# Kernel tuning notes

Measured on AMD Instinct MI355X. Metric: run time of the kernel, lower is better.

Reference implementation:

```python
import jax, jax.numpy as jnp
import numpy as np

DIM = 1024
HEADS = 16
DH = 64            # dim // heads
LOCAL_HEADS = 8
WINDOW = 128
NEG = -jnp.finfo(jnp.float32).max


def _look_around_kv(z, pad_value):
    # z: (b, h, nw, w, d) -> (b, h, nw, 3w, d); backward=1, forward=1 window
    nw = z.shape[2]
    zp = jnp.pad(z, ((0, 0), (0, 0), (1, 1), (0, 0), (0, 0)), constant_values=pad_value)
    return jnp.concatenate([zp[:, :, i:i + nw] for i in range(3)], axis=3)


def _local_attention(q, k, v, valid):
    # q,k,v: (b, h, t, d); valid: (b, t) True = keep (module passes ~input_mask)
    b, h, t, d = q.shape
    nw = t // WINDOW
    bucket = lambda z: z.reshape(b, h, nw, WINDOW, d)
    bq, bk, bv = bucket(q), bucket(k), bucket(v)
    bk = _look_around_kv(bk, 0.0)
    bv = _look_around_kv(bv, 0.0)
    # key position indices with -1 padding for out-of-range windows
    t_idx = jnp.arange(t, dtype=jnp.int32).reshape(nw, WINDOW)
    tp = jnp.pad(t_idx, ((1, 1), (0, 0)), constant_values=-1)
    bq_k = jnp.concatenate([tp[i:i + nw] for i in range(3)], axis=1)  # (nw, 3w)
    oob = (bq_k == -1)[None, None, :, None, :]                        # (1,1,nw,1,3w)
    # input mask pair: mq & mk
    vm = valid.reshape(b, nw, WINDOW)
    vmp = jnp.pad(vm, ((0, 0), (1, 1), (0, 0)), constant_values=False)
    vmk = jnp.concatenate([vmp[:, i:i + nw] for i in range(3)], axis=2)  # (b, nw, 3w)
    pair = vm[:, None, :, :, None] & vmk[:, None, :, None, :]            # (b,1,nw,w,3w)
    dots = jnp.einsum('bhnwd,bhnkd->bhnwk', bq, bk) * (d ** -0.5)
    dots = jnp.where(oob, NEG, dots)
    dots = jnp.where(pair, dots, NEG)
    attn = jax.nn.softmax(dots, axis=-1)
    out = jnp.einsum('bhnwk,bhnkd->bhnwd', attn, bv)
    return out.reshape(b, h, t, d)


def _linear_attn(q, k, v, valid):
    # q,k,v: (b, h, t, d); valid: (b, t) True = keep
    d = q.shape[-1]
    m = valid[:, None, :, None]
    k = jnp.where(m, k, NEG)
    v = jnp.where(m, v, 0.0)
    q = jax.nn.softmax(q, axis=-1) * (d ** -0.5)
    k = jax.nn.softmax(k, axis=-2)
    context = jnp.einsum('bhnd,bhne->bhde', k, v)
    return jnp.einsum('bhnd,bhde->bhne', q, context)


def setup_inputs() -> dict:
    key = jax.random.key(0)
    ks = jax.random.split(key, 7)
    b, t = 2, 4096
    x = jax.random.normal(ks[0], (b, t, DIM), dtype=jnp.float32)
    input_mask = jax.random.bernoulli(ks[1], 0.1, (b, t))  # True = padded token
    s = DIM ** -0.5
    Wq = jax.random.normal(ks[2], (DIM, HEADS * DH), jnp.float32) * s
    Wk = jax.random.normal(ks[3], (DIM, HEADS * DH), jnp.float32) * s
    Wv = jax.random.normal(ks[4], (DIM, HEADS * DH), jnp.float32) * s
    Wo = jax.random.normal(ks[5], (HEADS * DH, DIM), jnp.float32) * s
    bo = jax.random.normal(ks[6], (DIM,), jnp.float32) * 0.01
    return {"x": x, "input_mask": input_mask, "Wq": Wq, "Wk": Wk, "Wv": Wv, "Wo": Wo, "bo": bo}


def reference(x, input_mask, Wq, Wk, Wv, Wo, bo):
    b, t, _ = x.shape
    split_heads = lambda z: z.reshape(b, t, HEADS, DH).transpose(0, 2, 1, 3)
    q = split_heads(x @ Wq)
    k = split_heads(x @ Wk)
    v = split_heads(x @ Wv)
    valid = ~input_mask
    lq, gq = q[:, :LOCAL_HEADS], q[:, LOCAL_HEADS:]
    lk, gk = k[:, :LOCAL_HEADS], k[:, LOCAL_HEADS:]
    lv, gv = v[:, :LOCAL_HEADS], v[:, LOCAL_HEADS:]
    local_out = _local_attention(lq, lk, lv, valid)
    global_out = _linear_attn(gq, gk, gv, valid)
    attn = jnp.concatenate([local_out, global_out], axis=1)  # (b, h, t, d)
    attn = attn.transpose(0, 2, 1, 3).reshape(b, t, HEADS * DH)
    return attn @ Wo + bo
```

## Files before the change

### kernel.cpp

```cpp
#include <hip/hip_runtime.h>
#include <cstdint>
#include <cfloat>
#include <math.h>

typedef __bf16 bf16_t;
typedef __bf16 bf16x8 __attribute__((ext_vector_type(8)));
typedef __bf16 bf16x4 __attribute__((ext_vector_type(4)));
typedef float  f32x4  __attribute__((ext_vector_type(4)));
typedef unsigned int u32;

#define NEGF (-3.4028234663852886e38f)

static __device__ __forceinline__ f32x4 mfma16(bf16x8 a, bf16x8 b, f32x4 c) {
  return __builtin_amdgcn_mfma_f32_16x16x32_bf16(a, b, c, 0, 0, 0);
}
static __device__ __forceinline__ void gload_lds16(const bf16_t* g, bf16_t* l) {
  __builtin_amdgcn_global_load_lds((const __attribute__((address_space(1))) void*)g,
                                   (__attribute__((address_space(3))) void*)l, 16, 0, 0);
}

__global__ void k_prep(const uint8_t* __restrict__ mraw, uint8_t* __restrict__ valid) {
  __shared__ int f1, f3;
  int tid = threadIdx.x;
  if (tid == 0) { f1 = 0; f3 = 0; }
  __syncthreads();
  int l1 = 0, l3 = 0;
  for (int i = tid; i < 8192; i += 256) {
    uint8_t v = mraw[i];
    if (v) { int r = i & 3; if (r == 1 || r == 2) l1 = 1; if (r == 3) l3 = 1; }
  }
  if (l1) atomicOr(&f1, 1);
  if (l3) atomicOr(&f3, 1);
  __syncthreads();
  int layout = f1 ? 0 : (f3 ? 2 : 1);
  for (int i = tid; i < 8192; i += 256) {
    bool m;
    if (layout == 0)      m = mraw[i] != 0;
    else if (layout == 1) m = ((const int*)mraw)[i] != 0;
    else                  m = ((const float*)mraw)[i] != 0.0f;
    valid[i] = m ? (uint8_t)0 : (uint8_t)1;
  }
}

__global__ void k_cast_x(const float* __restrict__ x, bf16_t* __restrict__ xb) {
  int i = blockIdx.x * 256 + threadIdx.x;
  float4 v = ((const float4*)x)[i];
  bf16x4 o = { (bf16_t)v.x, (bf16_t)v.y, (bf16_t)v.z, (bf16_t)v.w };
  *(bf16x4*)(xb + (size_t)i * 4) = o;
}

__global__ void k_transw(const float* __restrict__ Wq, const float* __restrict__ Wk,
                         const float* __restrict__ Wv, const float* __restrict__ Wo,
                         bf16_t* __restrict__ WT, bf16_t* __restrict__ WoT) {
  __shared__ float tile[32][33];
  int z = blockIdx.z;
  const float* src = (z == 0) ? Wq : (z == 1) ? Wk : (z == 2) ? Wv : Wo;
  bf16_t* dst = (z < 3) ? (WT + (size_t)z * 1024 * 1024) : WoT;
  int x0 = blockIdx.x * 32, y0 = blockIdx.y * 32;
  int tx = threadIdx.x, ty = threadIdx.y;
  #pragma unroll
  for (int j = 0; j < 32; j += 8)
    tile[ty + j][tx] = src[(size_t)(y0 + ty + j) * 1024 + x0 + tx];
  __syncthreads();
  #pragma unroll
  for (int j = 0; j < 32; j += 8)
    dst[(size_t)(x0 + ty + j) * 1024 + y0 + tx] = (bf16_t)tile[tx][ty + j];
}

template<bool OUT_BF16>
__global__ __launch_bounds__(256, 2) void k_gemm(const bf16_t* __restrict__ A,
                                                 const bf16_t* __restrict__ Bt,
                                                 void* __restrict__ Cout,
                                                 const float* __restrict__ bias,
                                                 int M, int N, int K) {
  __shared__ __align__(16) uint8_t shmem[34816];
  bf16_t* As = (bf16_t*)shmem;
  bf16_t* Bs = As + 128 * 64;
  int nbn = N >> 7;
  int nwg = (M >> 7) * nbn;
  int per = nwg >> 3;
  int id  = blockIdx.x;
  int sw  = (id & 7) * per + (id >> 3);
  int mb = sw / nbn, nb = sw % nbn;

  const int tid = threadIdx.x;
  const int lane = tid & 63, wv = tid >> 6;
  const int c = lane & 15, g = lane >> 4;
  const size_t m0 = (size_t)mb * 128, n0 = (size_t)nb * 128;
  const int wm = (wv >> 1) * 64, wn = (wv & 1) * 64;

  f32x4 zero = {0.f, 0.f, 0.f, 0.f};
  f32x4 acc[4][4];
  #pragma unroll
  for (int m = 0; m < 4; ++m)
    #pragma unroll
    for (int n = 0; n < 4; ++n) acc[m][n] = zero;

  for (int kt = 0; kt < K; kt += 64) {
    if (kt) __syncthreads();
    #pragma unroll
    for (int p = 0; p < 4; ++p) {
      int seg = p * 256 + tid;
      int r = seg >> 3, s = seg & 7;
      int sc = (s ^ (r & 7)) * 8;
      gload_lds16(A + (m0 + r) * (size_t)K + kt + sc, As + seg * 8);
    }
    #pragma unroll
    for (int p = 0; p < 4; ++p) {
      int seg = p * 256 + tid;
      int r = seg >> 3, s = seg & 7;
      int sc = (s ^ (r & 7)) * 8;
      gload_lds16(Bt + (n0 + r) * (size_t)K + kt + sc, Bs + seg * 8);
    }
    __syncthreads();
    #pragma unroll
    for (int kk = 0; kk < 2; ++kk) {
      bf16x8 af[4], bfv[4];
      #pragma unroll
      for (int m = 0; m < 4; ++m) {
        int row = wm + m * 16 + c;
        int sl = (g + 4 * kk) ^ (row & 7);
        af[m] = *(const bf16x8*)(As + row * 64 + sl * 8);
      }
      #pragma unroll
      for (int n = 0; n < 4; ++n) {
        int row = wn + n * 16 + c;
        int sl = (g + 4 * kk) ^ (row & 7);
        bfv[n] = *(const bf16x8*)(Bs + row * 64 + sl * 8);
      }
      #pragma unroll
      for (int m = 0; m < 4; ++m)
        #pragma unroll
        for (int n = 0; n < 4; ++n)
          acc[m][n] = mfma16(af[m], bfv[n], acc[m][n]);
    }
  }

  __syncthreads();
  if (OUT_BF16) {
    bf16_t* L = (bf16_t*)shmem;
    #pragma unroll
    for (int m = 0; m < 4; ++m)
      #pragma unroll
      for (int n = 0; n < 4; ++n)
        #pragma unroll
        for (int i = 0; i < 4; ++i)
          L[(wm + m * 16 + 4 * g + i) * 136 + wn + n * 16 + c] = (bf16_t)acc[m][n][i];
    __syncthreads();
    bf16_t* C = (bf16_t*)Cout;
    #pragma unroll
    for (int p = 0; p < 8; ++p) {
      int idx = p * 2048 + tid * 8;
      int row = idx >> 7, col = idx & 127;
      bf16x8 v = *(const bf16x8*)(L + row * 136 + col);
      *(bf16x8*)(C + (m0 + row) * (size_t)N + n0 + col) = v;
    }
  } else {
    float* C = (float*)Cout;
    float* L = (float*)shmem;
    #pragma unroll
    for (int half = 0; half < 2; ++half) {
      if (half) __syncthreads();
      if ((wv >> 1) == half) {
        #pragma unroll
        for (int m = 0; m < 4; ++m)
          #pragma unroll
          for (int n = 0; n < 4; ++n)
            #pragma unroll
            for (int i = 0; i < 4; ++i)
              L[(m * 16 + 4 * g + i) * 132 + wn + n * 16 + c] = acc[m][n][i];
      }
      __syncthreads();
      #pragma unroll
      for (int p = 0; p < 8; ++p) {
        int lin = p * 1024 + tid * 4;
        int row = lin >> 7, col = lin & 127;
        float4 v = *(const float4*)(L + row * 132 + col);
        float4 bv = *(const float4*)(bias + n0 + col);
        v.x += bv.x; v.y += bv.y; v.z += bv.z; v.w += bv.w;
        *(float4*)(C + (m0 + half * 64 + row) * (size_t)N + n0 + col) = v;
      }
    }
  }
}

__global__ __launch_bounds__(512) void k_local(const bf16_t* __restrict__ qkv,
                                               const uint8_t* __restrict__ valid,
                                               bf16_t* __restrict__ attn) {
  __shared__ __align__(16) uint8_t smem[50688];
  bf16_t* Ks = (bf16_t*)smem;
  bf16_t* VT = (bf16_t*)smem;
  uint8_t* s_key = smem + 50176;
  uint8_t* s_q   = smem + 50560;

  int bid = blockIdx.x;
  int w = bid & 31, h = (bid >> 5) & 7, b = bid >> 8;
  int tid = threadIdx.x;
  const int lane = tid & 63, wv = tid >> 6;
  const int c = lane & 15, g = lane >> 4;
  const int tkbase = (w - 1) * 128;

  #pragma unroll
  for (int p = 0; p < 6; ++p) {
    int seg = p * 512 + tid;
    int r = seg >> 3, s = seg & 7;
    int tk = tkbase + r;
    bf16x8 v8 = { (bf16_t)0.f,(bf16_t)0.f,(bf16_t)0.f,(bf16_t)0.f,
                  (bf16_t)0.f,(bf16_t)0.f,(bf16_t)0.f,(bf16_t)0.f };
    if ((unsigned)tk < 4096u)
      v8 = *(const bf16x8*)(qkv + (size_t)(b * 4096 + tk) * 3072 + 1024 + h * 64 + s * 8);
    *(bf16x8*)(Ks + r * 64 + ((s ^ (r & 7)) * 8)) = v8;
  }
  if (tid < 384) {
    int tk = tkbase + tid;
    s_key[tid] = ((unsigned)tk < 4096u) ? valid[b * 4096 + tk] : (uint8_t)0;
  }
  if (tid < 128) s_q[tid] = valid[b * 4096 + w * 128 + tid];
  __syncthreads();

  int m0 = wv * 16;
  bf16x8 qa0, qa1;
  {
    const bf16_t* qrow = qkv + (size_t)(b * 4096 + w * 128 + m0 + c) * 3072 + h * 64;
    qa0 = *(const bf16x8*)(qrow + g * 8);
    qa1 = *(const bf16x8*)(qrow + 32 + g * 8);
  }
  f32x4 zero = {0.f, 0.f, 0.f, 0.f};
  f32x4 acc[24];
  #pragma unroll
  for (int nt = 0; nt < 24; ++nt) acc[nt] = zero;
  #pragma unroll
  for (int nt = 0; nt < 24; ++nt) {
    int n = nt * 16 + c;
    bf16x8 k0 = *(const bf16x8*)(Ks + n * 64 + ((g       ^ (n & 7)) * 8));
    bf16x8 k1 = *(const bf16x8*)(Ks + n * 64 + (((g + 4) ^ (n & 7)) * 8));
    acc[nt] = mfma16(k0, qa0, acc[nt]);
    acc[nt] = mfma16(k1, qa1, acc[nt]);
  }
  __syncthreads();

  {
    int e = tid & 63, tg = tid >> 6;
    #pragma unroll 8
    for (int j = 0; j < 48; ++j) {
      int r = tg * 48 + j;
      int tk = tkbase + r;
      bf16_t v = (bf16_t)0.f;
      if ((unsigned)tk < 4096u)
        v = qkv[(size_t)(b * 4096 + tk) * 3072 + 2048 + h * 64 + e];
      VT[e * 392 + r] = v;
    }
  }

  bool qv = s_q[m0 + c] != 0;
  #pragma unroll
  for (int nt = 0; nt < 24; ++nt) {
    u32 kv4 = *(const u32*)(s_key + nt * 16 + 4 * g);
    #pragma unroll
    for (int i = 0; i < 4; ++i) {
      bool kv = ((kv4 >> (8 * i)) & 255u) != 0u;
      acc[nt][i] = (qv && kv) ? acc[nt][i] * 0.125f : NEGF;
    }
  }
  float mx = NEGF;
  #pragma unroll
  for (int nt = 0; nt < 24; ++nt)
    #pragma unroll
    for (int i = 0; i < 4; ++i) mx = fmaxf(mx, acc[nt][i]);
  mx = fmaxf(mx, __shfl_xor(mx, 16, 64));
  mx = fmaxf(mx, __shfl_xor(mx, 32, 64));

  const int srcA = ((lane >> 4) & 1) * 32 + (lane & 15);
  const int srcB = srcA + 16;
  union Pk2 { bf16x4 h; uint2 u; };
  union Pk4 { uint4 u; bf16x8 h; };
  uint4 paU[12];
  #pragma unroll
  for (int ks = 0; ks < 12; ++ks) paU[ks] = make_uint4(0, 0, 0, 0);
  float sum = 0.f;
  #pragma unroll
  for (int nt = 0; nt < 24; ++nt) {
    Pk2 pk;
    #pragma unroll
    for (int i = 0; i < 4; ++i) {
      float e = __expf(acc[nt][i] - mx);
      sum += e;
      pk.h[i] = (bf16_t)e;
    }
    u32 a0 = (u32)__shfl((int)pk.u.x, srcA, 64);
    u32 a1 = (u32)__shfl((int)pk.u.y, srcA, 64);
    u32 b0 = (u32)__shfl((int)pk.u.x, srcB, 64);
    u32 b1 = (u32)__shfl((int)pk.u.y, srcB, 64);
    bool take = ((g >> 1) == (nt & 1));
    int ks = nt >> 1;
    paU[ks].x = take ? a0 : paU[ks].x;
    paU[ks].y = take ? a1 : paU[ks].y;
    paU[ks].z = take ? b0 : paU[ks].z;
    paU[ks].w = take ? b1 : paU[ks].w;
  }
  sum += __shfl_xor(sum, 16, 64);
  sum += __shfl_xor(sum, 32, 64);
  float inv = 1.f / sum;
  float invq[4];
  #pragma unroll
  for (int i = 0; i < 4; ++i) invq[i] = __shfl(inv, 4 * g + i, 64);
  __syncthreads();

  f32x4 o[4];
  #pragma unroll
  for (int n = 0; n < 4; ++n) o[n] = zero;
  #pragma unroll
  for (int ks = 0; ks < 12; ++ks) {
    Pk4 pa; pa.u = paU[ks];
    #pragma unroll
    for (int n = 0; n < 4; ++n) {
      bf16x8 vb = *(const bf16x8*)(VT + (n * 16 + c) * 392 + ks * 32 + g * 8);
      o[n] = mfma16(pa.h, vb, o[n]);
    }
  }
  size_t obase = (size_t)(b * 4096 + w * 128 + m0) * 1024 + h * 64;
  #pragma unroll
  for (int n = 0; n < 4; ++n)
    #pragma unroll
    for (int i = 0; i < 4; ++i)
      attn[obase + (size_t)(4 * g + i) * 1024 + n * 16 + c] = (bf16_t)(o[n][i] * invq[i]);
}

__global__ __launch_bounds__(256) void k_ctx1(const bf16_t* __restrict__ qkv,
                                              const uint8_t* __restrict__ valid,
                                              float* __restrict__ ctxp,
                                              float* __restrict__ sump) {
  int bid = blockIdx.x;
  int tc = bid & 15, h = (bid >> 4) & 7, b = bid >> 7;
  int tid = threadIdx.x;
  __shared__ float sk[128][64];
  __shared__ float sv[128][64];
  float a00=0,a01=0,a02=0,a03=0,a10=0,a11=0,a12=0,a13=0;
  float a20=0,a21=0,a22=0,a23=0,a30=0,a31=0,a32=0,a33=0;
  float s0=0, s1=0, s2=0, s3=0;
  int dg = tid >> 4, eg = tid & 15;
  for (int ch = 0; ch < 2; ++ch) {
    int t0 = tc * 256 + ch * 128;
    __syncthreads();
    for (int idx = tid; idx < 1024; idx += 256) {
      int r = idx >> 3, ss = idx & 7;
      int gt = b * 4096 + t0 + r;
      bool vld = valid[gt] != 0;
      bf16x8 k8 = *(const bf16x8*)(qkv + (size_t)gt * 3072 + 1024 + (8 + h) * 64 + ss * 8);
      bf16x8 v8 = *(const bf16x8*)(qkv + (size_t)gt * 3072 + 2048 + (8 + h) * 64 + ss * 8);
      #pragma unroll
      for (int j = 0; j < 8; ++j) {
        int dd = ss * 8 + j;
        sk[r][dd] = vld ? __expf((float)k8[j]) : 0.f;
        sv[r][dd] = vld ? (float)v8[j] : 0.f;
      }
    }
    __syncthreads();
    #pragma unroll 4
    for (int r = 0; r < 128; ++r) {
      float4 a = *(const float4*)&sk[r][dg * 4];
      float4 v = *(const float4*)&sv[r][eg * 4];
      a00 += a.x*v.x; a01 += a.x*v.y; a02 += a.x*v.z; a03 += a.x*v.w;
      a10 += a.y*v.x; a11 += a.y*v.y; a12 += a.y*v.z; a13 += a.y*v.w;
      a20 += a.z*v.x; a21 += a.z*v.y; a22 += a.z*v.z; a23 += a.z*v.w;
      a30 += a.w*v.x; a31 += a.w*v.y; a32 += a.w*v.z; a33 += a.w*v.w;
      s0 += a.x; s1 += a.y; s2 += a.z; s3 += a.w;
    }
  }
  float* dst = ctxp + (size_t)((b * 8 + h) * 16 + tc) * 4096 + (dg * 4) * 64 + eg * 4;
  *(float4*)(dst + 0)   = make_float4(a00, a01, a02, a03);
  *(float4*)(dst + 64)  = make_float4(a10, a11, a12, a13);
  *(float4*)(dst + 128) = make_float4(a20, a21, a22, a23);
  *(float4*)(dst + 192) = make_float4(a30, a31, a32, a33);
  if (eg == 0)
    *(float4*)(sump + (size_t)((b * 8 + h) * 16 + tc) * 64 + dg * 4) = make_float4(s0, s1, s2, s3);
}

__global__ __launch_bounds__(256) void k_ctx2(const float* __restrict__ ctxp,
                                              const float* __restrict__ sump,
                                              bf16_t* __restrict__ ctxT) {
  int bh = blockIdx.x;
  int tid = threadIdx.x;
  __shared__ float inv[64];
  if (tid < 64) {
    float s = 0.f;
    #pragma unroll
    for (int tc = 0; tc < 16; ++tc)
      s += sump[(size_t)(bh * 16 + tc) * 64 + tid];
    inv[tid] = 1.f / s;
  }
  __syncthreads();
  for (int p = 0; p < 16; ++p) {
    int lin = p * 256 + tid;
    int d = lin >> 6, e = lin & 63;
    float s = 0.f;
    #pragma unroll
    for (int tc = 0; tc < 16; ++tc)
      s += ctxp[(size_t)(bh * 16 + tc) * 4096 + lin];
    s *= inv[d];
    ctxT[(size_t)bh * 4096 + e * 64 + d] = (bf16_t)s;
  }
}

__global__ __launch_bounds__(256) void k_linout(const bf16_t* __restrict__ qkv,
                                                const bf16_t* __restrict__ ctxT,
                                                bf16_t* __restrict__ attn) {
  int bid = blockIdx.x;
  int tb2 = bid & 15, hg = (bid >> 4) & 7, b = bid >> 7;
  int tid = threadIdx.x;
  __shared__ bf16_t qs[256 * 72];
  __shared__ bf16_t cT[64 * 72];
  {
    int t = tb2 * 256 + tid;
    const bf16_t* qrow = qkv + (size_t)(b * 4096 + t) * 3072 + (8 + hg) * 64;
    float x[64];
    #pragma unroll
    for (int s8 = 0; s8 < 8; ++s8) {
      bf16x8 q8 = *(const bf16x8*)(qrow + s8 * 8);
      #pragma unroll
      for (int j = 0; j < 8; ++j) x[s8 * 8 + j] = (float)q8[j];
    }
    float m = x[0];
    #pragma unroll
    for (int i = 1; i < 64; ++i) m = fmaxf(m, x[i]);
    float sum = 0.f;
    #pragma unroll
    for (int i = 0; i < 64; ++i) { x[i] = __expf(x[i] - m); sum += x[i]; }
    float sc = 0.125f / sum;
    #pragma unroll
    for (int s8 = 0; s8 < 8; ++s8) {
      bf16x8 o8;
      #pragma unroll
      for (int j = 0; j < 8; ++j) o8[j] = (bf16_t)(x[s8 * 8 + j] * sc);
      *(bf16x8*)(qs + tid * 72 + s8 * 8) = o8;
    }
  }
  for (int idx = tid; idx < 512; idx += 256) {
    int r = idx >> 3, s = idx & 7;
    *(bf16x8*)(cT + r * 72 + s * 8) =
      *(const bf16x8*)(ctxT + (size_t)(b * 8 + hg) * 4096 + r * 64 + s * 8);
  }
  __syncthreads();
  int lane = tid & 63, wvv = tid >> 6;
  int c = lane & 15, g = lane >> 4;
  int m0w = wvv * 64;
  f32x4 zero = {0.f, 0.f, 0.f, 0.f};
  f32x4 acc[4][4];
  #pragma unroll
  for (int m = 0; m < 4; ++m)
    #pragma unroll
    for (int n = 0; n < 4; ++n) acc[m][n] = zero;
  #pragma unroll
  for (int kk = 0; kk < 2; ++kk) {
    bf16x8 af[4], bfv[4];
    #pragma unroll
    for (int m = 0; m < 4; ++m)
      af[m] = *(const bf16x8*)(qs + (m0w + m * 16 + c) * 72 + kk * 32 + g * 8);
    #pragma unroll
    for (int n = 0; n < 4; ++n)
      bfv[n] = *(const bf16x8*)(cT + (n * 16 + c) * 72 + kk * 32 + g * 8);
    #pragma unroll
    for (int m = 0; m < 4; ++m)
      #pragma unroll
      for (int n = 0; n < 4; ++n)
        acc[m][n] = mfma16(af[m], bfv[n], acc[m][n]);
  }
  size_t obase = (size_t)(b * 4096 + tb2 * 256 + m0w) * 1024 + (8 + hg) * 64;
  #pragma unroll
  for (int m = 0; m < 4; ++m)
    #pragma unroll
    for (int n = 0; n < 4; ++n)
      #pragma unroll
      for (int i = 0; i < 4; ++i)
        attn[obase + (size_t)(m * 16 + 4 * g + i) * 1024 + n * 16 + c] = (bf16_t)acc[m][n][i];
}

extern "C" void kernel_launch(void* const* d_in, const int* in_sizes, int n_in,
                              void* d_out, int out_size, void* d_ws, size_t ws_size,
                              hipStream_t stream) {
  const float*   x    = (const float*)d_in[0];
  const uint8_t* mraw = (const uint8_t*)d_in[1];
  const float*   Wq   = (const float*)d_in[2];
  const float*   Wk   = (const float*)d_in[3];
  const float*   Wv   = (const float*)d_in[4];
  const float*   Wo   = (const float*)d_in[5];
  const float*   bo   = (const float*)d_in[6];
  uint8_t* ws = (uint8_t*)d_ws;

  uint8_t* valid = ws;
  bf16_t*  xb    = (bf16_t*)(ws + 8192);
  bf16_t*  WT    = (bf16_t*)(ws + 16785408);
  bf16_t*  WoT   = (bf16_t*)(ws + 23076864);
  bf16_t*  qkv   = (bf16_t*)(ws + 25174016);
  bf16_t*  attn  = (bf16_t*)(ws + 75505664);
  float*   ctxp  = (float*)(ws + 8192);
  float*   sump  = (float*)(ws + 4202496);
  bf16_t*  ctxT  = (bf16_t*)(ws + 4268032);

  k_prep<<<1, 256, 0, stream>>>(mraw, valid);
  k_cast_x<<<8192, 256, 0, stream>>>(x, xb);
  k_transw<<<dim3(32, 32, 4), dim3(32, 8), 0, stream>>>(Wq, Wk, Wv, Wo, WT, WoT);
  k_gemm<true><<<1536, 256, 0, stream>>>(xb, WT, (void*)qkv, nullptr, 8192, 3072, 1024);
  k_local<<<512, 512, 0, stream>>>(qkv, valid, attn);
  k_ctx1<<<256, 256, 0, stream>>>(qkv, valid, ctxp, sump);
  k_ctx2<<<16, 256, 0, stream>>>(ctxp, sump, ctxT);
  k_linout<<<256, 256, 0, stream>>>(qkv, ctxT, attn);
  k_gemm<false><<<512, 256, 0, stream>>>(attn, WoT, d_out, bo, 8192, 1024, 1024);
}
```

Before: 218.8 us.

## Triple-buffer GEMM with 256x128 tiles and fuse prep kernels into one launch

Replaces the single-buffered 128x128 GEMM with a 512-thread, 256x128-tile kernel. It keeps three LDS stages and prefetches two k-tiles ahead, splitting each k-tile into two half-steps with raw barriers, explicit waitcnts and setprio around the MFMA bursts. The aim is to hide global-to-LDS load latency behind compute and to improve reuse per workgroup. It also merges the mask-prep, x-cast and weight-transpose kernels into one launch to cut launch overhead. The cost is 144KB of LDS per block, which limits occupancy to one block per CU, plus fragile hand-tuned waitcnt counts.

```diff
diff --git a/kernel.cpp b/kernel.cpp
--- a/kernel.cpp
+++ b/kernel.cpp
@@ -18,66 +18,81 @@
   __builtin_amdgcn_global_load_lds((const __attribute__((address_space(1))) void*)g,
                                    (__attribute__((address_space(3))) void*)l, 16, 0, 0);
 }
-
-__global__ void k_prep(const uint8_t* __restrict__ mraw, uint8_t* __restrict__ valid) {
-  __shared__ int f1, f3;
+static __device__ __forceinline__ void barrier_raw() {
+  __builtin_amdgcn_sched_barrier(0);
+  asm volatile("" ::: "memory");
+  __builtin_amdgcn_s_barrier();
+  __builtin_amdgcn_sched_barrier(0);
+  asm volatile("" ::: "memory");
+}
+
+__global__ __launch_bounds__(256) void k_prep_all(const float* __restrict__ x,
+                                                  const uint8_t* __restrict__ mraw,
+                                                  const float* __restrict__ Wq,
+                                                  const float* __restrict__ Wk,
+                                                  const float* __restrict__ Wv,
+                                                  const float* __restrict__ Wo,
+                                                  bf16_t* __restrict__ xb,
+                                                  bf16_t* __restrict__ WT,
+                                                  bf16_t* __restrict__ WoT,
+                                                  uint8_t* __restrict__ valid) {
+  int bid = blockIdx.x;
   int tid = threadIdx.x;
-  if (tid == 0) { f1 = 0; f3 = 0; }
-  __syncthreads();
-  int l1 = 0, l3 = 0;
-  for (int i = tid; i < 8192; i += 256) {
-    uint8_t v = mraw[i];
-    if (v) { int r = i & 3; if (r == 1 || r == 2) l1 = 1; if (r == 3) l3 = 1; }
-  }
-  if (l1) atomicOr(&f1, 1);
-  if (l3) atomicOr(&f3, 1);
-  __syncthreads();
-  int layout = f1 ? 0 : (f3 ? 2 : 1);
-  for (int i = tid; i < 8192; i += 256) {
-    bool m;
-    if (layout == 0)      m = mraw[i] != 0;
-    else if (layout == 1) m = ((const int*)mraw)[i] != 0;
-    else                  m = ((const float*)mraw)[i] != 0.0f;
-    valid[i] = m ? (uint8_t)0 : (uint8_t)1;
-  }
-}
-
-__global__ void k_cast_x(const float* __restrict__ x, bf16_t* __restrict__ xb) {
-  int i = blockIdx.x * 256 + threadIdx.x;
-  float4 v = ((const float4*)x)[i];
-  bf16x4 o = { (bf16_t)v.x, (bf16_t)v.y, (bf16_t)v.z, (bf16_t)v.w };
-  *(bf16x4*)(xb + (size_t)i * 4) = o;
-}
-
-__global__ void k_transw(const float* __restrict__ Wq, const float* __restrict__ Wk,
-                         const float* __restrict__ Wv, const float* __restrict__ Wo,
-                         bf16_t* __restrict__ WT, bf16_t* __restrict__ WoT) {
-  __shared__ float tile[32][33];
-  int z = blockIdx.z;
-  const float* src = (z == 0) ? Wq : (z == 1) ? Wk : (z == 2) ? Wv : Wo;
-  bf16_t* dst = (z < 3) ? (WT + (size_t)z * 1024 * 1024) : WoT;
-  int x0 = blockIdx.x * 32, y0 = blockIdx.y * 32;
-  int tx = threadIdx.x, ty = threadIdx.y;
-  #pragma unroll
-  for (int j = 0; j < 32; j += 8)
-    tile[ty + j][tx] = src[(size_t)(y0 + ty + j) * 1024 + x0 + tx];
-  __syncthreads();
-  #pragma unroll
-  for (int j = 0; j < 32; j += 8)
-    dst[(size_t)(x0 + ty + j) * 1024 + y0 + tx] = (bf16_t)tile[tx][ty + j];
+  if (bid < 8192) {
+    int i = bid * 256 + tid;
+    float4 v = ((const float4*)x)[i];
+    bf16x4 o = { (bf16_t)v.x, (bf16_t)v.y, (bf16_t)v.z, (bf16_t)v.w };
+    *(bf16x4*)(xb + (size_t)i * 4) = o;
+  } else if (bid < 12288) {
+    __shared__ float tile[32][33];
+    int zz = bid - 8192;
+    int z = zz >> 10, rem = zz & 1023;
+    int bx = rem & 31, by = rem >> 5;
+    const float* src = (z == 0) ? Wq : (z == 1) ? Wk : (z == 2) ? Wv : Wo;
+    bf16_t* dst = (z < 3) ? (WT + (size_t)z * 1024 * 1024) : WoT;
+    int x0 = bx * 32, y0 = by * 32;
+    int tx = tid & 31, ty = tid >> 5;
+    #pragma unroll
+    for (int j = 0; j < 32; j += 8)
+      tile[ty + j][tx] = src[(size_t)(y0 + ty + j) * 1024 + x0 + tx];
+    __syncthreads();
+    #pragma unroll
+    for (int j = 0; j < 32; j += 8)
+      dst[(size_t)(x0 + ty + j) * 1024 + y0 + tx] = (bf16_t)tile[tx][ty + j];
+  } else {
+    __shared__ int f1, f3;
+    if (tid == 0) { f1 = 0; f3 = 0; }
+    __syncthreads();
+    int l1 = 0, l3 = 0;
+    for (int i = tid; i < 8192; i += 256) {
+      uint8_t v = mraw[i];
+      if (v) { int r = i & 3; if (r == 1 || r == 2) l1 = 1; if (r == 3) l3 = 1; }
+    }
+    if (l1) atomicOr(&f1, 1);
+    if (l3) atomicOr(&f3, 1);
+    __syncthreads();
+    int layout = f1 ? 0 : (f3 ? 2 : 1);
+    for (int i = tid; i < 8192; i += 256) {
+      bool m;
+      if (layout == 0)      m = mraw[i] != 0;
+      else if (layout == 1) m = ((const int*)mraw)[i] != 0;
+      else                  m = ((const float*)mraw)[i] != 0.0f;
+      valid[i] = m ? (uint8_t)0 : (uint8_t)1;
+    }
+  }
 }
 
 template<bool OUT_BF16>
-__global__ __launch_bounds__(256, 2) void k_gemm(const bf16_t* __restrict__ A,
-                                                 const bf16_t* __restrict__ Bt,
-                                                 void* __restrict__ Cout,
-                                                 const float* __restrict__ bias,
-                                                 int M, int N, int K) {
-  __shared__ __align__(16) uint8_t shmem[34816];
-  bf16_t* As = (bf16_t*)shmem;
-  bf16_t* Bs = As + 128 * 64;
+__global__ __launch_bounds__(512) void k_gemm3(const bf16_t* __restrict__ A,
+                                               const bf16_t* __restrict__ Bt,
+                                               void* __restrict__ Cout,
+                                               const float* __restrict__ bias,
+                                               int M, int N, int K) {
+  __shared__ __align__(16) uint8_t shmem[147456];
+  bf16_t* lds = (bf16_t*)shmem;
+  const int NT = K >> 6;
   int nbn = N >> 7;
-  int nwg = (M >> 7) * nbn;
+  int nwg = (M >> 8) * nbn;
   int per = nwg >> 3;
   int id  = blockIdx.x;
   int sw  = (id & 7) * per + (id >> 3);
@@ -86,8 +101,23 @@
   const int tid = threadIdx.x;
   const int lane = tid & 63, wv = tid >> 6;
   const int c = lane & 15, g = lane >> 4;
-  const size_t m0 = (size_t)mb * 128, n0 = (size_t)nb * 128;
-  const int wm = (wv >> 1) * 64, wn = (wv & 1) * 64;
+  const size_t m0 = (size_t)mb * 256, n0 = (size_t)nb * 128;
+  const int wr = wv >> 1, wc = wv & 1;
+
+  auto stageA = [&](int t, int p) {
+    int seg = p * 512 + tid;
+    int r = seg >> 3, s = seg & 7;
+    int sc = (s ^ (r & 7)) * 8;
+    gload_lds16(A + (m0 + r) * (size_t)K + (t << 6) + sc,
+                lds + (t % 3) * 24576 + seg * 8);
+  };
+  auto stageB = [&](int t, int p) {
+    int seg = p * 512 + tid;
+    int r = seg >> 3, s = seg & 7;
+    int sc = (s ^ (r & 7)) * 8;
+    gload_lds16(Bt + (n0 + r) * (size_t)K + (t << 6) + sc,
+                lds + (t % 3) * 24576 + 16384 + seg * 8);
+  };
 
   f32x4 zero = {0.f, 0.f, 0.f, 0.f};
   f32x4 acc[4][4];
@@ -96,43 +126,70 @@
     #pragma unroll
     for (int n = 0; n < 4; ++n) acc[m][n] = zero;
 
-  for (int kt = 0; kt < K; kt += 64) {
-    if (kt) __syncthreads();
-    #pragma unroll
-    for (int p = 0; p < 4; ++p) {
-      int seg = p * 256 + tid;
-      int r = seg >> 3, s = seg & 7;
-      int sc = (s ^ (r & 7)) * 8;
-      gload_lds16(A + (m0 + r) * (size_t)K + kt + sc, As + seg * 8);
-    }
-    #pragma unroll
-    for (int p = 0; p < 4; ++p) {
-      int seg = p * 256 + tid;
-      int r = seg >> 3, s = seg & 7;
-      int sc = (s ^ (r & 7)) * 8;
-      gload_lds16(Bt + (n0 + r) * (size_t)K + kt + sc, Bs + seg * 8);
-    }
-    __syncthreads();
-    #pragma unroll
-    for (int kk = 0; kk < 2; ++kk) {
-      bf16x8 af[4], bfv[4];
-      #pragma unroll
-      for (int m = 0; m < 4; ++m) {
-        int row = wm + m * 16 + c;
-        int sl = (g + 4 * kk) ^ (row & 7);
-        af[m] = *(const bf16x8*)(As + row * 64 + sl * 8);
-      }
-      #pragma unroll
-      for (int n = 0; n < 4; ++n) {
-        int row = wn + n * 16 + c;
-        int sl = (g + 4 * kk) ^ (row & 7);
-        bfv[n] = *(const bf16x8*)(Bs + row * 64 + sl * 8);
-      }
-      #pragma unroll
-      for (int m = 0; m < 4; ++m)
-        #pragma unroll
-        for (int n = 0; n < 4; ++n)
-          acc[m][n] = mfma16(af[m], bfv[n], acc[m][n]);
+  #pragma unroll
+  for (int p = 0; p < 4; ++p) stageA(0, p);
+  stageB(0, 0); stageB(0, 1);
+  #pragma unroll
+  for (int p = 0; p < 4; ++p) stageA(1, p);
+  stageB(1, 0); stageB(1, 1);
+  asm volatile("s_waitcnt vmcnt(6)" ::: "memory");
+  barrier_raw();
+
+  for (int t = 0; t < NT; ++t) {
+    const bf16_t* As = lds + (t % 3) * 24576;
+    const bf16_t* Bs = As + 16384;
+    bool pf = (t + 2) < NT;
+
+    bf16x8 af[4], bfv[4];
+    #pragma unroll
+    for (int m = 0; m < 4; ++m) {
+      int row = wr * 64 + m * 16 + c;
+      af[m] = *(const bf16x8*)(As + row * 64 + ((g ^ (row & 7)) * 8));
+    }
+    #pragma unroll
+    for (int n = 0; n < 4; ++n) {
+      int row = wc * 64 + n * 16 + c;
+      bfv[n] = *(const bf16x8*)(Bs + row * 64 + ((g ^ (row & 7)) * 8));
+    }
+    if (pf) { stageA(t + 2, 0); stageA(t + 2, 1); stageA(t + 2, 2); }
+    barrier_raw();
+    asm volatile("s_waitcnt lgkmcnt(0)" ::: "memory");
+    __builtin_amdgcn_sched_barrier(0);
+    __builtin_amdgcn_s_setprio(1);
+    #pragma unroll
+    for (int m = 0; m < 4; ++m)
+      #pragma unroll
+      for (int n = 0; n < 4; ++n)
+        acc[m][n] = mfma16(af[m], bfv[n], acc[m][n]);
+    __builtin_amdgcn_s_setprio(0);
+    barrier_raw();
+
+    #pragma unroll
+    for (int m = 0; m < 4; ++m) {
+      int row = wr * 64 + m * 16 + c;
+      af[m] = *(const bf16x8*)(As + row * 64 + (((g + 4) ^ (row & 7)) * 8));
+    }
+    #pragma unroll
+    for (int n = 0; n < 4; ++n) {
+      int row = wc * 64 + n * 16 + c;
+      bfv[n] = *(const bf16x8*)(Bs + row * 64 + (((g + 4) ^ (row & 7)) * 8));
+    }
+    if (pf) { stageA(t + 2, 3); stageB(t + 2, 0); stageB(t + 2, 1); }
+    barrier_raw();
+    asm volatile("s_waitcnt lgkmcnt(0)" ::: "memory");
+    __builtin_amdgcn_sched_barrier(0);
+    __builtin_amdgcn_s_setprio(1);
+    #pragma unroll
+    for (int m = 0; m < 4; ++m)
+      #pragma unroll
+      for (int n = 0; n < 4; ++n)
+        acc[m][n] = mfma16(af[m], bfv[n], acc[m][n]);
+    __builtin_amdgcn_s_setprio(0);
+
+    if (t < NT - 1) {
+      if (pf) asm volatile("s_waitcnt vmcnt(6)" ::: "memory");
+      else    asm volatile("s_waitcnt vmcnt(0)" ::: "memory");
+      barrier_raw();
     }
   }
 
@@ -145,12 +202,12 @@
       for (int n = 0; n < 4; ++n)
         #pragma unroll
         for (int i = 0; i < 4; ++i)
-          L[(wm + m * 16 + 4 * g + i) * 136 + wn + n * 16 + c] = (bf16_t)acc[m][n][i];
+          L[(wr * 64 + m * 16 + 4 * g + i) * 136 + wc * 64 + n * 16 + c] = (bf16_t)acc[m][n][i];
     __syncthreads();
     bf16_t* C = (bf16_t*)Cout;
     #pragma unroll
     for (int p = 0; p < 8; ++p) {
-      int idx = p * 2048 + tid * 8;
+      int idx = p * 4096 + tid * 8;
       int row = idx >> 7, col = idx & 127;
       bf16x8 v = *(const bf16x8*)(L + row * 136 + col);
       *(bf16x8*)(C + (m0 + row) * (size_t)N + n0 + col) = v;
@@ -161,24 +218,24 @@
     #pragma unroll
     for (int half = 0; half < 2; ++half) {
       if (half) __syncthreads();
-      if ((wv >> 1) == half) {
+      if ((wr >> 1) == half) {
         #pragma unroll
         for (int m = 0; m < 4; ++m)
           #pragma unroll
           for (int n = 0; n < 4; ++n)
             #pragma unroll
             for (int i = 0; i < 4; ++i)
-              L[(m * 16 + 4 * g + i) * 132 + wn + n * 16 + c] = acc[m][n][i];
+              L[((wr & 1) * 64 + m * 16 + 4 * g + i) * 132 + wc * 64 + n * 16 + c] = acc[m][n][i];
       }
       __syncthreads();
       #pragma unroll
       for (int p = 0; p < 8; ++p) {
-        int lin = p * 1024 + tid * 4;
+        int lin = p * 2048 + tid * 4;
         int row = lin >> 7, col = lin & 127;
         float4 v = *(const float4*)(L + row * 132 + col);
         float4 bv = *(const float4*)(bias + n0 + col);
         v.x += bv.x; v.y += bv.y; v.z += bv.z; v.w += bv.w;
-        *(float4*)(C + (m0 + half * 64 + row) * (size_t)N + n0 + col) = v;
+        *(float4*)(C + (m0 + half * 128 + row) * (size_t)N + n0 + col) = v;
       }
     }
   }
@@ -497,13 +554,11 @@
   float*   sump  = (float*)(ws + 4202496);
   bf16_t*  ctxT  = (bf16_t*)(ws + 4268032);
 
-  k_prep<<<1, 256, 0, stream>>>(mraw, valid);
-  k_cast_x<<<8192, 256, 0, stream>>>(x, xb);
-  k_transw<<<dim3(32, 32, 4), dim3(32, 8), 0, stream>>>(Wq, Wk, Wv, Wo, WT, WoT);
-  k_gemm<true><<<1536, 256, 0, stream>>>(xb, WT, (void*)qkv, nullptr, 8192, 3072, 1024);
+  k_prep_all<<<12289, 256, 0, stream>>>(x, mraw, Wq, Wk, Wv, Wo, xb, WT, WoT, valid);
+  k_gemm3<true><<<768, 512, 0, stream>>>(xb, WT, (void*)qkv, nullptr, 8192, 3072, 1024);
   k_local<<<512, 512, 0, stream>>>(qkv, valid, attn);
   k_ctx1<<<256, 256, 0, stream>>>(qkv, valid, ctxp, sump);
   k_ctx2<<<16, 256, 0, stream>>>(ctxp, sump, ctxT);
   k_linout<<<256, 256, 0, stream>>>(qkv, ctxT, attn);
-  k_gemm<false><<<512, 256, 0, stream>>>(attn, WoT, d_out, bo, 8192, 1024, 1024);
-}
+  k_gemm3<false><<<256, 512, 0, stream>>>(attn, WoT, d_out, bo, 8192, 1024, 1024);
+}
```

Result: slower. 224.2 us (+2.5%).

## Merge prep kernels and local/linear-context kernels into single launches, retile GEMM order

Applied to the files above, without the earlier changes.

The mask preparation, the x cast and the weight transpose are merged into one launch that dispatches on block index. The local windowed attention and the linear-attention context partial sums are merged into one 768-block launch, so the two independent workloads can run side by side. The context branch now stages 64-row chunks and uses only 256 of 512 threads for compute. The GEMM block swizzle is replaced with a fixed 8x8 tile grouping aimed at L2 reuse. This trades fewer launches and gaps between kernels for idle threads in the context path and a swizzle that assumes M=8192.

```diff
diff --git a/kernel.cpp b/kernel.cpp
--- a/kernel.cpp
+++ b/kernel.cpp
@@ -19,52 +19,60 @@
                                    (__attribute__((address_space(3))) void*)l, 16, 0, 0);
 }
 
-__global__ void k_prep(const uint8_t* __restrict__ mraw, uint8_t* __restrict__ valid) {
-  __shared__ int f1, f3;
+__global__ __launch_bounds__(256) void k_prep_all(const float* __restrict__ x,
+                                                  const uint8_t* __restrict__ mraw,
+                                                  const float* __restrict__ Wq,
+                                                  const float* __restrict__ Wk,
+                                                  const float* __restrict__ Wv,
+                                                  const float* __restrict__ Wo,
+                                                  bf16_t* __restrict__ xb,
+                                                  bf16_t* __restrict__ WT,
+                                                  bf16_t* __restrict__ WoT,
+                                                  uint8_t* __restrict__ valid) {
+  int bid = blockIdx.x;
   int tid = threadIdx.x;
-  if (tid == 0) { f1 = 0; f3 = 0; }
-  __syncthreads();
-  int l1 = 0, l3 = 0;
-  for (int i = tid; i < 8192; i += 256) {
-    uint8_t v = mraw[i];
-    if (v) { int r = i & 3; if (r == 1 || r == 2) l1 = 1; if (r == 3) l3 = 1; }
-  }
-  if (l1) atomicOr(&f1, 1);
-  if (l3) atomicOr(&f3, 1);
-  __syncthreads();
-  int layout = f1 ? 0 : (f3 ? 2 : 1);
-  for (int i = tid; i < 8192; i += 256) {
-    bool m;
-    if (layout == 0)      m = mraw[i] != 0;
-    else if (layout == 1) m = ((const int*)mraw)[i] != 0;
-    else                  m = ((const float*)mraw)[i] != 0.0f;
-    valid[i] = m ? (uint8_t)0 : (uint8_t)1;
-  }
-}
-
-__global__ void k_cast_x(const float* __restrict__ x, bf16_t* __restrict__ xb) {
-  int i = blockIdx.x * 256 + threadIdx.x;
-  float4 v = ((const float4*)x)[i];
-  bf16x4 o = { (bf16_t)v.x, (bf16_t)v.y, (bf16_t)v.z, (bf16_t)v.w };
-  *(bf16x4*)(xb + (size_t)i * 4) = o;
-}
-
-__global__ void k_transw(const float* __restrict__ Wq, const float* __restrict__ Wk,
-                         const float* __restrict__ Wv, const float* __restrict__ Wo,
-                         bf16_t* __restrict__ WT, bf16_t* __restrict__ WoT) {
-  __shared__ float tile[32][33];
-  int z = blockIdx.z;
-  const float* src = (z == 0) ? Wq : (z == 1) ? Wk : (z == 2) ? Wv : Wo;
-  bf16_t* dst = (z < 3) ? (WT + (size_t)z * 1024 * 1024) : WoT;
-  int x0 = blockIdx.x * 32, y0 = blockIdx.y * 32;
-  int tx = threadIdx.x, ty = threadIdx.y;
-  #pragma unroll
-  for (int j = 0; j < 32; j += 8)
-    tile[ty + j][tx] = src[(size_t)(y0 + ty + j) * 1024 + x0 + tx];
-  __syncthreads();
-  #pragma unroll
-  for (int j = 0; j < 32; j += 8)
-    dst[(size_t)(x0 + ty + j) * 1024 + y0 + tx] = (bf16_t)tile[tx][ty + j];
+  if (bid < 8192) {
+    int i = bid * 256 + tid;
+    float4 v = ((const float4*)x)[i];
+    bf16x4 o = { (bf16_t)v.x, (bf16_t)v.y, (bf16_t)v.z, (bf16_t)v.w };
+    *(bf16x4*)(xb + (size_t)i * 4) = o;
+  } else if (bid < 12288) {
+    __shared__ float tile[32][33];
+    int zz = bid - 8192;
+    int z = zz >> 10, rem = zz & 1023;
+    int bx = rem & 31, by = rem >> 5;
+    const float* src = (z == 0) ? Wq : (z == 1) ? Wk : (z == 2) ? Wv : Wo;
+    bf16_t* dst = (z < 3) ? (WT + (size_t)z * 1024 * 1024) : WoT;
+    int x0 = bx * 32, y0 = by * 32;
+    int tx = tid & 31, ty = tid >> 5;
+    #pragma unroll
+    for (int j = 0; j < 32; j += 8)
+      tile[ty + j][tx] = src[(size_t)(y0 + ty + j) * 1024 + x0 + tx];
+    __syncthreads();
+    #pragma unroll
+    for (int j = 0; j < 32; j += 8)
+      dst[(size_t)(x0 + ty + j) * 1024 + y0 + tx] = (bf16_t)tile[tx][ty + j];
+  } else {
+    __shared__ int f1, f3;
+    if (tid == 0) { f1 = 0; f3 = 0; }
+    __syncthreads();
+    int l1 = 0, l3 = 0;
+    for (int i = tid; i < 8192; i += 256) {
+      uint8_t v = mraw[i];
+      if (v) { int r = i & 3; if (r == 1 || r == 2) l1 = 1; if (r == 3) l3 = 1; }
+    }
+    if (l1) atomicOr(&f1, 1);
+    if (l3) atomicOr(&f3, 1);
+    __syncthreads();
+    int layout = f1 ? 0 : (f3 ? 2 : 1);
+    for (int i = tid; i < 8192; i += 256) {
+      bool m;
+      if (layout == 0)      m = mraw[i] != 0;
+      else if (layout == 1) m = ((const int*)mraw)[i] != 0;
+      else                  m = ((const float*)mraw)[i] != 0.0f;
+      valid[i] = m ? (uint8_t)0 : (uint8_t)1;
+    }
+  }
 }
 
 template<bool OUT_BF16>
@@ -76,12 +84,11 @@
   __shared__ __align__(16) uint8_t shmem[34816];
   bf16_t* As = (bf16_t*)shmem;
   bf16_t* Bs = As + 128 * 64;
-  int nbn = N >> 7;
-  int nwg = (M >> 7) * nbn;
-  int per = nwg >> 3;
   int id  = blockIdx.x;
-  int sw  = (id & 7) * per + (id >> 3);
-  int mb = sw / nbn, nb = sw % nbn;
+  int seq = id >> 3;
+  int nbg = seq >> 6, inner = seq & 63;
+  int mb = ((id & 7) << 3) + (inner >> 3);
+  int nb = (nbg << 3) + (inner & 7);
 
   const int tid = threadIdx.x;
   const int lane = tid & 63, wv = tid >> 6;
@@ -184,196 +191,200 @@
   }
 }
 
-__global__ __launch_bounds__(512) void k_local(const bf16_t* __restrict__ qkv,
-                                               const uint8_t* __restrict__ valid,
-                                               bf16_t* __restrict__ attn) {
-  __shared__ __align__(16) uint8_t smem[50688];
-  bf16_t* Ks = (bf16_t*)smem;
-  bf16_t* VT = (bf16_t*)smem;
-  uint8_t* s_key = smem + 50176;
-  uint8_t* s_q   = smem + 50560;
-
-  int bid = blockIdx.x;
-  int w = bid & 31, h = (bid >> 5) & 7, b = bid >> 8;
-  int tid = threadIdx.x;
-  const int lane = tid & 63, wv = tid >> 6;
-  const int c = lane & 15, g = lane >> 4;
-  const int tkbase = (w - 1) * 128;
-
-  #pragma unroll
-  for (int p = 0; p < 6; ++p) {
-    int seg = p * 512 + tid;
-    int r = seg >> 3, s = seg & 7;
-    int tk = tkbase + r;
-    bf16x8 v8 = { (bf16_t)0.f,(bf16_t)0.f,(bf16_t)0.f,(bf16_t)0.f,
-                  (bf16_t)0.f,(bf16_t)0.f,(bf16_t)0.f,(bf16_t)0.f };
-    if ((unsigned)tk < 4096u)
-      v8 = *(const bf16x8*)(qkv + (size_t)(b * 4096 + tk) * 3072 + 1024 + h * 64 + s * 8);
-    *(bf16x8*)(Ks + r * 64 + ((s ^ (r & 7)) * 8)) = v8;
-  }
-  if (tid < 384) {
-    int tk = tkbase + tid;
-    s_key[tid] = ((unsigned)tk < 4096u) ? valid[b * 4096 + tk] : (uint8_t)0;
-  }
-  if (tid < 128) s_q[tid] = valid[b * 4096 + w * 128 + tid];
-  __syncthreads();
-
-  int m0 = wv * 16;
-  bf16x8 qa0, qa1;
-  {
-    const bf16_t* qrow = qkv + (size_t)(b * 4096 + w * 128 + m0 + c) * 3072 + h * 64;
-    qa0 = *(const bf16x8*)(qrow + g * 8);
-    qa1 = *(const bf16x8*)(qrow + 32 + g * 8);
-  }
-  f32x4 zero = {0.f, 0.f, 0.f, 0.f};
-  f32x4 acc[24];
-  #pragma unroll
-  for (int nt = 0; nt < 24; ++nt) acc[nt] = zero;
-  #pragma unroll
-  for (int nt = 0; nt < 24; ++nt) {
-    int n = nt * 16 + c;
-    bf16x8 k0 = *(const bf16x8*)(Ks + n * 64 + ((g       ^ (n & 7)) * 8));
-    bf16x8 k1 = *(const bf16x8*)(Ks + n * 64 + (((g + 4) ^ (n & 7)) * 8));
-    acc[nt] = mfma16(k0, qa0, acc[nt]);
-    acc[nt] = mfma16(k1, qa1, acc[nt]);
-  }
-  __syncthreads();
-
-  {
-    int e = tid & 63, tg = tid >> 6;
-    #pragma unroll 8
-    for (int j = 0; j < 48; ++j) {
-      int r = tg * 48 + j;
-      int tk = tkbase + r;
-      bf16_t v = (bf16_t)0.f;
-      if ((unsigned)tk < 4096u)
-        v = qkv[(size_t)(b * 4096 + tk) * 3072 + 2048 + h * 64 + e];
-      VT[e * 392 + r] = v;
-    }
-  }
-
-  bool qv = s_q[m0 + c] != 0;
-  #pragma unroll
-  for (int nt = 0; nt < 24; ++nt) {
-    u32 kv4 = *(const u32*)(s_key + nt * 16 + 4 * g);
-    #pragma unroll
-    for (int i = 0; i < 4; ++i) {
-      bool kv = ((kv4 >> (8 * i)) & 255u) != 0u;
-      acc[nt][i] = (qv && kv) ? acc[nt][i] * 0.125f : NEGF;
-    }
-  }
-  float mx = NEGF;
-  #pragma unroll
-  for (int nt = 0; nt < 24; ++nt)
-    #pragma unroll
-    for (int i = 0; i < 4; ++i) mx = fmaxf(mx, acc[nt][i]);
-  mx = fmaxf(mx, __shfl_xor(mx, 16, 64));
-  mx = fmaxf(mx, __shfl_xor(mx, 32, 64));
-
-  const int srcA = ((lane >> 4) & 1) * 32 + (lane & 15);
-  const int srcB = srcA + 16;
-  union Pk2 { bf16x4 h; uint2 u; };
-  union Pk4 { uint4 u; bf16x8 h; };
-  uint4 paU[12];
-  #pragma unroll
-  for (int ks = 0; ks < 12; ++ks) paU[ks] = make_uint4(0, 0, 0, 0);
-  float sum = 0.f;
-  #pragma unroll
-  for (int nt = 0; nt < 24; ++nt) {
-    Pk2 pk;
-    #pragma unroll
-    for (int i = 0; i < 4; ++i) {
-      float e = __expf(acc[nt][i] - mx);
-      sum += e;
-      pk.h[i] = (bf16_t)e;
-    }
-    u32 a0 = (u32)__shfl((int)pk.u.x, srcA, 64);
-    u32 a1 = (u32)__shfl((int)pk.u.y, srcA, 64);
-    u32 b0 = (u32)__shfl((int)pk.u.x, srcB, 64);
-    u32 b1 = (u32)__shfl((int)pk.u.y, srcB, 64);
-    bool take = ((g >> 1) == (nt & 1));
-    int ks = nt >> 1;
-    paU[ks].x = take ? a0 : paU[ks].x;
-    paU[ks].y = take ? a1 : paU[ks].y;
-    paU[ks].z = take ? b0 : paU[ks].z;
-    paU[ks].w = take ? b1 : paU[ks].w;
-  }
-  sum += __shfl_xor(sum, 16, 64);
-  sum += __shfl_xor(sum, 32, 64);
-  float inv = 1.f / sum;
-  float invq[4];
-  #pragma unroll
-  for (int i = 0; i < 4; ++i) invq[i] = __shfl(inv, 4 * g + i, 64);
-  __syncthreads();
-
-  f32x4 o[4];
-  #pragma unroll
-  for (int n = 0; n < 4; ++n) o[n] = zero;
-  #pragma unroll
-  for (int ks = 0; ks < 12; ++ks) {
-    Pk4 pa; pa.u = paU[ks];
-    #pragma unroll
-    for (int n = 0; n < 4; ++n) {
-      bf16x8 vb = *(const bf16x8*)(VT + (n * 16 + c) * 392 + ks * 32 + g * 8);
-      o[n] = mfma16(pa.h, vb, o[n]);
-    }
-  }
-  size_t obase = (size_t)(b * 4096 + w * 128 + m0) * 1024 + h * 64;
-  #pragma unroll
-  for (int n = 0; n < 4; ++n)
-    #pragma unroll
-    for (int i = 0; i < 4; ++i)
-      attn[obase + (size_t)(4 * g + i) * 1024 + n * 16 + c] = (bf16_t)(o[n][i] * invq[i]);
-}
-
-__global__ __launch_bounds__(256) void k_ctx1(const bf16_t* __restrict__ qkv,
+__global__ __launch_bounds__(512) void k_attn(const bf16_t* __restrict__ qkv,
                                               const uint8_t* __restrict__ valid,
+                                              bf16_t* __restrict__ attn,
                                               float* __restrict__ ctxp,
                                               float* __restrict__ sump) {
+  __shared__ __align__(16) uint8_t smem[50688];
   int bid = blockIdx.x;
-  int tc = bid & 15, h = (bid >> 4) & 7, b = bid >> 7;
   int tid = threadIdx.x;
-  __shared__ float sk[128][64];
-  __shared__ float sv[128][64];
-  float a00=0,a01=0,a02=0,a03=0,a10=0,a11=0,a12=0,a13=0;
-  float a20=0,a21=0,a22=0,a23=0,a30=0,a31=0,a32=0,a33=0;
-  float s0=0, s1=0, s2=0, s3=0;
-  int dg = tid >> 4, eg = tid & 15;
-  for (int ch = 0; ch < 2; ++ch) {
-    int t0 = tc * 256 + ch * 128;
-    __syncthreads();
-    for (int idx = tid; idx < 1024; idx += 256) {
-      int r = idx >> 3, ss = idx & 7;
-      int gt = b * 4096 + t0 + r;
-      bool vld = valid[gt] != 0;
-      bf16x8 k8 = *(const bf16x8*)(qkv + (size_t)gt * 3072 + 1024 + (8 + h) * 64 + ss * 8);
-      bf16x8 v8 = *(const bf16x8*)(qkv + (size_t)gt * 3072 + 2048 + (8 + h) * 64 + ss * 8);
-      #pragma unroll
-      for (int j = 0; j < 8; ++j) {
-        int dd = ss * 8 + j;
-        sk[r][dd] = vld ? __expf((float)k8[j]) : 0.f;
-        sv[r][dd] = vld ? (float)v8[j] : 0.f;
-      }
-    }
-    __syncthreads();
-    #pragma unroll 4
-    for (int r = 0; r < 128; ++r) {
-      float4 a = *(const float4*)&sk[r][dg * 4];
-      float4 v = *(const float4*)&sv[r][eg * 4];
-      a00 += a.x*v.x; a01 += a.x*v.y; a02 += a.x*v.z; a03 += a.x*v.w;
-      a10 += a.y*v.x; a11 += a.y*v.y; a12 += a.y*v.z; a13 += a.y*v.w;
-      a20 += a.z*v.x; a21 += a.z*v.y; a22 += a.z*v.z; a23 += a.z*v.w;
-      a30 += a.w*v.x; a31 += a.w*v.y; a32 += a.w*v.z; a33 += a.w*v.w;
-      s0 += a.x; s1 += a.y; s2 += a.z; s3 += a.w;
-    }
-  }
-  float* dst = ctxp + (size_t)((b * 8 + h) * 16 + tc) * 4096 + (dg * 4) * 64 + eg * 4;
-  *(float4*)(dst + 0)   = make_float4(a00, a01, a02, a03);
-  *(float4*)(dst + 64)  = make_float4(a10, a11, a12, a13);
-  *(float4*)(dst + 128) = make_float4(a20, a21, a22, a23);
-  *(float4*)(dst + 192) = make_float4(a30, a31, a32, a33);
-  if (eg == 0)
-    *(float4*)(sump + (size_t)((b * 8 + h) * 16 + tc) * 64 + dg * 4) = make_float4(s0, s1, s2, s3);
+
+  if (bid < 512) {
+    bf16_t* Ks = (bf16_t*)smem;
+    bf16_t* VT = (bf16_t*)smem;
+    uint8_t* s_key = smem + 50176;
+    uint8_t* s_q   = smem + 50560;
+
+    int w = bid & 31, h = (bid >> 5) & 7, b = bid >> 8;
+    const int lane = tid & 63, wv = tid >> 6;
+    const int c = lane & 15, g = lane >> 4;
+    const int tkbase = (w - 1) * 128;
+
+    #pragma unroll
+    for (int p = 0; p < 6; ++p) {
+      int seg = p * 512 + tid;
+      int r = seg >> 3, s = seg & 7;
+      int tk = tkbase + r;
+      bf16x8 v8 = { (bf16_t)0.f,(bf16_t)0.f,(bf16_t)0.f,(bf16_t)0.f,
+                    (bf16_t)0.f,(bf16_t)0.f,(bf16_t)0.f,(bf16_t)0.f };
+      if ((unsigned)tk < 4096u)
+        v8 = *(const bf16x8*)(qkv + (size_t)(b * 4096 + tk) * 3072 + 1024 + h * 64 + s * 8);
+      *(bf16x8*)(Ks + r * 64 + ((s ^ (r & 7)) * 8)) = v8;
+    }
+    if (tid < 384) {
+      int tk = tkbase + tid;
+      s_key[tid] = ((unsigned)tk < 4096u) ? valid[b * 4096 + tk] : (uint8_t)0;
+    }
+    if (tid < 128) s_q[tid] = valid[b * 4096 + w * 128 + tid];
+    __syncthreads();
+
+    int m0 = wv * 16;
+    bf16x8 qa0, qa1;
+    {
+      const bf16_t* qrow = qkv + (size_t)(b * 4096 + w * 128 + m0 + c) * 3072 + h * 64;
+      qa0 = *(const bf16x8*)(qrow + g * 8);
+      qa1 = *(const bf16x8*)(qrow + 32 + g * 8);
+    }
+    f32x4 zero = {0.f, 0.f, 0.f, 0.f};
+    f32x4 acc[24];
+    #pragma unroll
+    for (int nt = 0; nt < 24; ++nt) acc[nt] = zero;
+    #pragma unroll
+    for (int nt = 0; nt < 24; ++nt) {
+      int n = nt * 16 + c;
+      bf16x8 k0 = *(const bf16x8*)(Ks + n * 64 + ((g       ^ (n & 7)) * 8));
+      bf16x8 k1 = *(const bf16x8*)(Ks + n * 64 + (((g + 4) ^ (n & 7)) * 8));
+      acc[nt] = mfma16(k0, qa0, acc[nt]);
+      acc[nt] = mfma16(k1, qa1, acc[nt]);
+    }
+    __syncthreads();
+
+    {
+      int e = tid & 63, tg = tid >> 6;
+      #pragma unroll 8
+      for (int j = 0; j < 48; ++j) {
+        int r = tg * 48 + j;
+        int tk = tkbase + r;
+        bf16_t v = (bf16_t)0.f;
+        if ((unsigned)tk < 4096u)
+          v = qkv[(size_t)(b * 4096 + tk) * 3072 + 2048 + h * 64 + e];
+        VT[e * 392 + r] = v;
+      }
+    }
+
+    bool qv = s_q[m0 + c] != 0;
+    #pragma unroll
+    for (int nt = 0; nt < 24; ++nt) {
+      u32 kv4 = *(const u32*)(s_key + nt * 16 + 4 * g);
+      #pragma unroll
+      for (int i = 0; i < 4; ++i) {
+        bool kv = ((kv4 >> (8 * i)) & 255u) != 0u;
+        acc[nt][i] = (qv && kv) ? acc[nt][i] * 0.125f : NEGF;
+      }
+    }
+    float mx = NEGF;
+    #pragma unroll
+    for (int nt = 0; nt < 24; ++nt)
+      #pragma unroll
+      for (int i = 0; i < 4; ++i) mx = fmaxf(mx, acc[nt][i]);
+    mx = fmaxf(mx, __shfl_xor(mx, 16, 64));
+    mx = fmaxf(mx, __shfl_xor(mx, 32, 64));
+
+    const int srcA = ((lane >> 4) & 1) * 32 + (lane & 15);
+    const int srcB = srcA + 16;
+    union Pk2 { bf16x4 h; uint2 u; };
+    union Pk4 { uint4 u; bf16x8 h; };
+    uint4 paU[12];
+    #pragma unroll
+    for (int ks = 0; ks < 12; ++ks) paU[ks] = make_uint4(0, 0, 0, 0);
+    float sum = 0.f;
+    #pragma unroll
+    for (int nt = 0; nt < 24; ++nt) {
+      Pk2 pk;
+      #pragma unroll
+      for (int i = 0; i < 4; ++i) {
+        float e = __expf(acc[nt][i] - mx);
+        sum += e;
+        pk.h[i] = (bf16_t)e;
+      }
+      u32 a0 = (u32)__shfl((int)pk.u.x, srcA, 64);
+      u32 a1 = (u32)__shfl((int)pk.u.y, srcA, 64);
+      u32 b0 = (u32)__shfl((int)pk.u.x, srcB, 64);
+      u32 b1 = (u32)__shfl((int)pk.u.y, srcB, 64);
+      bool take = ((g >> 1) == (nt & 1));
+      int ks = nt >> 1;
+      paU[ks].x = take ? a0 : paU[ks].x;
+      paU[ks].y = take ? a1 : paU[ks].y;
+      paU[ks].z = take ? b0 : paU[ks].z;
+      paU[ks].w = take ? b1 : paU[ks].w;
+    }
+    sum += __shfl_xor(sum, 16, 64);
+    sum += __shfl_xor(sum, 32, 64);
+    float inv = 1.f / sum;
+    float invq[4];
+    #pragma unroll
+    for (int i = 0; i < 4; ++i) invq[i] = __shfl(inv, 4 * g + i, 64);
+    __syncthreads();
+
+    f32x4 o[4];
+    #pragma unroll
+    for (int n = 0; n < 4; ++n) o[n] = zero;
+    #pragma unroll
+    for (int ks = 0; ks < 12; ++ks) {
+      Pk4 pa; pa.u = paU[ks];
+      #pragma unroll
+      for (int n = 0; n < 4; ++n) {
+        bf16x8 vb = *(const bf16x8*)(VT + (n * 16 + c) * 392 + ks * 32 + g * 8);
+        o[n] = mfma16(pa.h, vb, o[n]);
+      }
+    }
+    size_t obase = (size_t)(b * 4096 + w * 128 + m0) * 1024 + h * 64;
+    #pragma unroll
+    for (int n = 0; n < 4; ++n)
+      #pragma unroll
+      for (int i = 0; i < 4; ++i)
+        attn[obase + (size_t)(4 * g + i) * 1024 + n * 16 + c] = (bf16_t)(o[n][i] * invq[i]);
+  } else {
+    int bid2 = bid - 512;
+    int tc = bid2 & 15, h = (bid2 >> 4) & 7, b = bid2 >> 7;
+    float* sk = (float*)smem;
+    float* sv = sk + 64 * 64;
+    float a00=0,a01=0,a02=0,a03=0,a10=0,a11=0,a12=0,a13=0;
+    float a20=0,a21=0,a22=0,a23=0,a30=0,a31=0,a32=0,a33=0;
+    float s0=0, s1=0, s2=0, s3=0;
+    int dg = tid >> 4, eg = tid & 15;
+    for (int ch = 0; ch < 4; ++ch) {
+      int t0 = tc * 256 + ch * 64;
+      __syncthreads();
+      {
+        int idx = tid;
+        int r = idx >> 3, ss = idx & 7;
+        int gt = b * 4096 + t0 + r;
+        bool vld = valid[gt] != 0;
+        bf16x8 k8 = *(const bf16x8*)(qkv + (size_t)gt * 3072 + 1024 + (8 + h) * 64 + ss * 8);
+        bf16x8 v8 = *(const bf16x8*)(qkv + (size_t)gt * 3072 + 2048 + (8 + h) * 64 + ss * 8);
+        #pragma unroll
+        for (int j = 0; j < 8; ++j) {
+          int dd = ss * 8 + j;
+          sk[r * 64 + dd] = vld ? __expf((float)k8[j]) : 0.f;
+          sv[r * 64 + dd] = vld ? (float)v8[j] : 0.f;
+        }
+      }
+      __syncthreads();
+      if (tid < 256) {
+        #pragma unroll 4
+        for (int r = 0; r < 64; ++r) {
+          float4 a = *(const float4*)(sk + r * 64 + dg * 4);
+          float4 v = *(const float4*)(sv + r * 64 + eg * 4);
+          a00 += a.x*v.x; a01 += a.x*v.y; a02 += a.x*v.z; a03 += a.x*v.w;
+          a10 += a.y*v.x; a11 += a.y*v.y; a12 += a.y*v.z; a13 += a.y*v.w;
+          a20 += a.z*v.x; a21 += a.z*v.y; a22 += a.z*v.z; a23 += a.z*v.w;
+          a30 += a.w*v.x; a31 += a.w*v.y; a32 += a.w*v.z; a33 += a.w*v.w;
+          s0 += a.x; s1 += a.y; s2 += a.z; s3 += a.w;
+        }
+      }
+    }
+    if (tid < 256) {
+      float* dst = ctxp + (size_t)((b * 8 + h) * 16 + tc) * 4096 + (dg * 4) * 64 + eg * 4;
+      *(float4*)(dst + 0)   = make_float4(a00, a01, a02, a03);
+      *(float4*)(dst + 64)  = make_float4(a10, a11, a12, a13);
+      *(float4*)(dst + 128) = make_float4(a20, a21, a22, a23);
+      *(float4*)(dst + 192) = make_float4(a30, a31, a32, a33);
+      if (eg == 0)
+        *(float4*)(sump + (size_t)((b * 8 + h) * 16 + tc) * 64 + dg * 4) = make_float4(s0, s1, s2, s3);
+    }
+  }
 }
 
 __global__ __launch_bounds__(256) void k_ctx2(const float* __restrict__ ctxp,
@@ -497,12 +508,9 @@
   float*   sump  = (float*)(ws + 4202496);
   bf16_t*  ctxT  = (bf16_t*)(ws + 4268032);
 
-  k_prep<<<1, 256, 0, stream>>>(mraw, valid);
-  k_cast_x<<<8192, 256, 0, stream>>>(x, xb);
-  k_transw<<<dim3(32, 32, 4), dim3(32, 8), 0, stream>>>(Wq, Wk, Wv, Wo, WT, WoT);
+  k_prep_all<<<12289, 256, 0, stream>>>(x, mraw, Wq, Wk, Wv, Wo, xb, WT, WoT, valid);
   k_gemm<true><<<1536, 256, 0, stream>>>(xb, WT, (void*)qkv, nullptr, 8192, 3072, 1024);
-  k_local<<<512, 512, 0, stream>>>(qkv, valid, attn);
-  k_ctx1<<<256, 256, 0, stream>>>(qkv, valid, ctxp, sump);
+  k_attn<<<768, 512, 0, stream>>>(qkv, valid, attn, ctxp, sump);
   k_ctx2<<<16, 256, 0, stream>>>(ctxp, sump, ctxT);
   k_linout<<<256, 256, 0, stream>>>(qkv, ctxT, attn);
   k_gemm<false><<<512, 256, 0, stream>>>(attn, WoT, d_out, bo, 8192, 1024, 1024);
```

Result: faster. 207.2 us (-5.3%).
